# Performance work log

Hardware: AMD Instinct MI355X
Metric: run time of the kernel (lower is better)

Reference implementation:

```python
import jax, jax.numpy as jnp
import numpy as np

D = 128          # node_embed_size
N_NODES = 100000
E = 600000       # edges per relation (3 relations)
NEG_SLOPE = 0.01 # F.leaky_relu default


def setup_inputs() -> dict:
    key = jax.random.key(0)
    ks = jax.random.split(key, 17)
    s = 1.0 / np.sqrt(D)
    inp = {
        "N": jax.random.normal(ks[0], (N_NODES, D), jnp.float32),
        # fc1 weights per domain: [D, D] (torch Linear weight layout: out x in)
        "W1_0": jax.random.normal(ks[1], (D, D), jnp.float32) * s,
        "W1_1": jax.random.normal(ks[2], (D, D), jnp.float32) * s,
        "W1_2": jax.random.normal(ks[3], (D, D), jnp.float32) * s,
        # fc2 weights per domain: [1, 2D]
        "w2_0": jax.random.normal(ks[4], (1, 2 * D), jnp.float32) * s,
        "w2_1": jax.random.normal(ks[5], (1, 2 * D), jnp.float32) * s,
        "w2_2": jax.random.normal(ks[6], (1, 2 * D), jnp.float32) * s,
        "Wq": jax.random.normal(ks[7], (D, D), jnp.float32) * s,
        "Wk": jax.random.normal(ks[8], (D, D), jnp.float32) * s,
        "Wv": jax.random.normal(ks[9], (D, D), jnp.float32) * s,
        "src0": jax.random.randint(ks[10], (E,), 0, N_NODES, jnp.int32),
        "dst0": jax.random.randint(ks[11], (E,), 0, N_NODES, jnp.int32),
        "src1": jax.random.randint(ks[12], (E,), 0, N_NODES, jnp.int32),
        "dst1": jax.random.randint(ks[13], (E,), 0, N_NODES, jnp.int32),
        "src2": jax.random.randint(ks[14], (E,), 0, N_NODES, jnp.int32),
        "dst2": jax.random.randint(ks[15], (E,), 0, N_NODES, jnp.int32),
        "target_idx": 0,
    }
    return inp


def _leaky(x):
    return jnp.where(x >= 0, x, NEG_SLOPE * x)


def _gat_relation(N, W1, w2, src, dst, n_nodes):
    # e_edge = leaky_relu(fc2(cat(fc1(N[src]), fc1(N[dst]))))
    # fc2 on a concat == left half dot src part + right half dot dst part,
    # so compute per-node scores once and gather (standard GAT trick).
    d = N.shape[1]
    h = N @ W1.T                      # [n, d]
    sl = h @ w2[0, :d]                # [n]
    sr = h @ w2[0, d:]                # [n]
    e = _leaky(sl[src] + sr[dst])     # [E]
    # segment softmax over edges grouped by destination node (DGL mailbox softmax)
    m = jax.ops.segment_max(e, dst, num_segments=n_nodes)   # [n], -inf for empty
    ex = jnp.exp(e - m[dst])                                 # [E]
    den = jax.ops.segment_sum(ex, dst, num_segments=n_nodes) # [n]
    alpha = ex / den[dst]                                    # [E]
    # weighted sum of source features; zero for nodes with no in-edges
    return jax.ops.segment_sum(alpha[:, None] * N[src], dst, num_segments=n_nodes)


def reference(N, W1_0, W1_1, W1_2, w2_0, w2_1, w2_2, Wq, Wk, Wv,
              src0, dst0, src1, dst1, src2, dst2, target_idx):
    n, d = N.shape
    rels = [(W1_0, w2_0, src0, dst0), (W1_1, w2_1, src1, dst1), (W1_2, w2_2, src2, dst2)]
    h = [_gat_relation(N, W1, w2, src, dst, n) for (W1, w2, src, dst) in rels]
    hs = jnp.stack(h)                         # [3, n, d]
    q = h[target_idx] @ Wq.T                  # [n, d]
    k = jnp.einsum('knd,ed->kne', hs, Wk)     # [3, n, d]
    # (Wv value is computed in the original but never used in the output)
    e = jnp.einsum('nd,knd->nk', q, k) / jnp.sqrt(jnp.asarray(d, N.dtype))  # [n, 3]
    a = jax.nn.softmax(e, axis=1)             # [n, 3]
    Np = jnp.einsum('nk,knd->nd', a, hs)      # [n, d]
    return Np
```

## Files before the change

kernel.cpp:

```cpp
#include <hip/hip_runtime.h>
#include <hip/hip_bf16.h>
#include <math.h>

#define DD 128

typedef __attribute__((ext_vector_type(8))) short short8;
typedef __attribute__((ext_vector_type(4))) float f32x4;

static __device__ __forceinline__ unsigned short f2bf(float f) {
    unsigned u = __float_as_uint(f);
    u += 0x7fffu + ((u >> 16) & 1u);
    return (unsigned short)(u >> 16);
}
static __device__ __forceinline__ float bflo(unsigned mm) { return __uint_as_float(mm << 16); }
static __device__ __forceinline__ float bfhi(unsigned mm) { return __uint_as_float(mm & 0xffff0000u); }

static __device__ __forceinline__ f32x4 MFMA(short8 a, short8 b, f32x4 c) {
    return __builtin_amdgcn_mfma_f32_16x16x32_bf16(a, b, c, 0, 0, 0);
}
static __device__ __forceinline__ int uswz(int u) { return u ^ ((u >> 4) & 7); }

__global__ void k_fill(float* __restrict__ out, float v, int n) {
    int i = blockIdx.x * 256 + threadIdx.x;
    if (i < n) out[i] = v;
}

__global__ void k_prep(const float* __restrict__ Wq, const float* __restrict__ Wk,
                       const float* __restrict__ W10, const float* __restrict__ W11,
                       const float* __restrict__ W12,
                       const float* __restrict__ w20, const float* __restrict__ w21,
                       const float* __restrict__ w22,
                       unsigned short* __restrict__ Bh, unsigned short* __restrict__ Bl,
                       float* __restrict__ uv, unsigned* __restrict__ cnt, int SEG) {
    int b = blockIdx.x, j = threadIdx.x;
    if (b < DD) {
        float acc = 0.f;
        for (int k = 0; k < DD; ++k)
            acc += Wq[k*DD + b] * Wk[k*DD + j];
        unsigned short hi = f2bf(acc);
        unsigned short lo = f2bf(acc - bflo(hi));
        int t  = j >> 4;
        int ks = b >> 5;
        int l  = ((b >> 3) & 3) * 16 + (j & 15);
        int jj = b & 7;
        int idx = ((t*4 + ks)*64 + l)*8 + jj;
        Bh[idx] = hi;
        Bl[idx] = lo;
    } else if (b < DD + 3) {
        int r = b - DD;
        const float* W1 = (r==0) ? W10 : (r==1 ? W11 : W12);
        const float* w2 = (r==0) ? w20 : (r==1 ? w21 : w22);
        float u = 0.f, v = 0.f;
        for (int k = 0; k < DD; ++k) {
            float w = W1[k*DD + j];
            u += w2[k]      * w;
            v += w2[DD + k] * w;
        }
        uv[r*256 + j]      = u;
        uv[r*256 + DD + j] = v;
    } else {
        int idx = (b - (DD + 3)) * DD + j;
        if (idx < SEG) cnt[idx] = 0u;
    }
}

__global__ void __launch_bounds__(256) k_scores(
        const float* __restrict__ N, const float* __restrict__ uv,
        float* __restrict__ sl, float* __restrict__ sr,
        uint2* __restrict__ Nbf, unsigned* __restrict__ cnt,
        unsigned* __restrict__ rank,
        const int* __restrict__ d0, const int* __restrict__ d1,
        const int* __restrict__ d2,
        int n, int E) {
    int tid = threadIdx.x;
    int g = blockIdx.x * 256 + tid;
    if (g < 3*E) {
        int r = (g >= 2*E) ? 2 : (g >= E ? 1 : 0);
        int e = g - r*E;
        const int* Dd = (r==0) ? d0 : (r==1 ? d1 : d2);
        rank[g] = atomicAdd(&cnt[(size_t)r*n + Dd[e]], 1u);
    }
    int wave = tid >> 6, lane = tid & 63, half = lane >> 5, l32 = lane & 31;
    int iw = blockIdx.x * 8 + wave * 2 + half;
    if (iw >= n && blockIdx.x * 8 >= n) return;
    int i = (iw < n) ? iw : (n - 1);
    float4 nv = ((const float4*)N)[(size_t)i * 32 + l32];
    if (iw < n) {
        uint2 pk;
        pk.x = (unsigned)f2bf(nv.x) | ((unsigned)f2bf(nv.y) << 16);
        pk.y = (unsigned)f2bf(nv.z) | ((unsigned)f2bf(nv.w) << 16);
        Nbf[(size_t)iw * 32 + l32] = pk;
    }
    const float4* UV4 = (const float4*)uv;
    float acc[6];
#pragma unroll
    for (int r = 0; r < 3; ++r) {
        float4 u = UV4[r*64 + l32];
        float4 v = UV4[r*64 + 32 + l32];
        acc[2*r]   = nv.x*u.x + nv.y*u.y + nv.z*u.z + nv.w*u.w;
        acc[2*r+1] = nv.x*v.x + nv.y*v.y + nv.z*v.z + nv.w*v.w;
    }
#pragma unroll
    for (int o = 16; o; o >>= 1) {
#pragma unroll
        for (int q = 0; q < 6; ++q) acc[q] += __shfl_xor(acc[q], o);
    }
    if (l32 == 0 && iw < n) {
#pragma unroll
        for (int r = 0; r < 3; ++r) {
            sl[(size_t)r*n + iw] = acc[2*r];
            sr[(size_t)r*n + iw] = acc[2*r+1];
        }
    }
}

__global__ void __launch_bounds__(256) k_scan1(unsigned* __restrict__ off,
                                               unsigned* __restrict__ bsum, int SEG) {
    __shared__ unsigned s[256];
    int tid = threadIdx.x;
    int i = blockIdx.x * 256 + tid;
    unsigned v = (i < SEG) ? off[i] : 0u;
    s[tid] = v; __syncthreads();
#pragma unroll
    for (int o = 1; o < 256; o <<= 1) {
        unsigned a = (tid >= o) ? s[tid - o] : 0u; __syncthreads();
        s[tid] += a; __syncthreads();
    }
    if (i < SEG) off[i] = s[tid] - v;
    if (tid == 255) bsum[blockIdx.x] = s[255];
}

__global__ void __launch_bounds__(256) k_scan2(unsigned* __restrict__ bsum, int nb) {
    __shared__ unsigned s[256];
    __shared__ unsigned carry;
    int tid = threadIdx.x;
    if (tid == 0) carry = 0u;
    for (int base = 0; base < nb; base += 256) {
        int i = base + tid;
        unsigned v = (i < nb) ? bsum[i] : 0u;
        __syncthreads();
        s[tid] = v; __syncthreads();
#pragma unroll
        for (int o = 1; o < 256; o <<= 1) {
            unsigned a = (tid >= o) ? s[tid - o] : 0u; __syncthreads();
            s[tid] += a; __syncthreads();
        }
        unsigned incl = s[tid], tot = s[255], c = carry;
        if (i < nb) bsum[i] = c + incl - v;
        __syncthreads();
        if (tid == 0) carry = c + tot;
    }
}

__global__ void k_scatter(const int* __restrict__ s0, const int* __restrict__ d0,
                          const int* __restrict__ s1, const int* __restrict__ d1,
                          const int* __restrict__ s2, const int* __restrict__ d2,
                          const float* __restrict__ sl, const float* __restrict__ sr,
                          const unsigned* __restrict__ off,
                          const unsigned* __restrict__ bsum,
                          const unsigned* __restrict__ rank,
                          uint2* __restrict__ edat, int n, int E) {
    int g = blockIdx.x * 256 + threadIdx.x;
    if (g >= 3*E) return;
    int r = (g >= 2*E) ? 2 : (g >= E ? 1 : 0);
    int e = g - r*E;
    const int* S  = (r==0) ? s0 : (r==1 ? s1 : s2);
    const int* Dd = (r==0) ? d0 : (r==1 ? d1 : d2);
    int si = S[e], di = Dd[e];
    int seg = r*n + di;
    float x = sl[(size_t)r*n + si] + sr[seg];
    x = (x >= 0.f) ? x : 0.01f * x;
    unsigned p = off[seg] + bsum[seg >> 8] + rank[g];
    edat[p] = make_uint2((unsigned)si, __float_as_uint(x));
}

__global__ void __launch_bounds__(512, 8) k_node(
        const uint4* __restrict__ Nbf,
        const uint4* __restrict__ B4h, const uint4* __restrict__ B4l,
        const unsigned* __restrict__ off,
        const unsigned* __restrict__ bsum,
        const uint2* __restrict__ edat,
        const int* __restrict__ tgt,
        float* __restrict__ out, int n, int TOT) {
    __shared__ uint4 afrag[2][256];
    __shared__ float Tl[16*132];
    int tid = threadIdx.x;
    int wave = tid >> 6, lane = tid & 63;
    int half = lane >> 5;
    int l32 = lane & 31;
    int g2 = (lane >> 4) & 1;
    int l16 = lane & 15;
    int nid = wave * 2 + half;
    int iw = blockIdx.x * 16 + nid;
    int i = (iw < n) ? iw : (n - 1);
    int t = tgt[0];
    t = (t < 0) ? 0 : (t > 2 ? 2 : t);
    int SEG = 3*n;

    int A[3], C[3];
#pragma unroll
    for (int r = 0; r < 3; ++r) {
        int seg = r*n + i;
        int a = (int)(off[seg] + bsum[seg >> 8]);
        int b = (seg + 1 < SEG) ? (int)(off[seg+1] + bsum[(seg+1) >> 8]) : TOT;
        A[r] = a; C[r] = b - a;
    }

    float m_[3], inv_[3];
#pragma unroll
    for (int r = 0; r < 3; ++r) {
        int cc = C[r];
        float m, s;
        if (cc <= 32) {
            float x = (l32 < cc) ? __uint_as_float(edat[A[r] + l32].y) : -INFINITY;
            m = x;
#pragma unroll
            for (int o = 16; o; o >>= 1) m = fmaxf(m, __shfl_xor(m, o));
            s = (l32 < cc) ? __expf(x - m) : 0.f;
#pragma unroll
            for (int o = 16; o; o >>= 1) s += __shfl_xor(s, o);
        } else {
            m = -INFINITY;
            for (int j = A[r] + l32; j < A[r] + cc; j += 32)
                m = fmaxf(m, __uint_as_float(edat[j].y));
#pragma unroll
            for (int o = 16; o; o >>= 1) m = fmaxf(m, __shfl_xor(m, o));
            s = 0.f;
            for (int j = A[r] + l32; j < A[r] + cc; j += 32)
                s += __expf(__uint_as_float(edat[j].y) - m);
#pragma unroll
            for (int o = 16; o; o >>= 1) s += __shfl_xor(s, o);
        }
        m_[r] = m; inv_[r] = 1.f / s;
    }

    float hr[3][8];
#pragma unroll
    for (int r = 0; r < 3; ++r) {
        float h[8] = {0.f,0.f,0.f,0.f,0.f,0.f,0.f,0.f};
        int cc = C[r], a = A[r];
        float mm = m_[r], iv = inv_[r];
        for (int p = 0; p < cc; p += 4) {
            int i0 = p + g2, i1 = p + 2 + g2;
            int e0 = (i0 < cc) ? i0 : cc - 1;
            int e1 = (i1 < cc) ? i1 : cc - 1;
            uint2 d0 = edat[a + e0];
            uint2 d1 = edat[a + e1];
            uint4 v0 = Nbf[(size_t)d0.x * 16 + l16];
            uint4 v1 = Nbf[(size_t)d1.x * 16 + l16];
            float a0 = (i0 < cc) ? __expf(__uint_as_float(d0.y) - mm) * iv : 0.f;
            float a1 = (i1 < cc) ? __expf(__uint_as_float(d1.y) - mm) * iv : 0.f;
            h[0] += a0*bflo(v0.x) + a1*bflo(v1.x);
            h[1] += a0*bfhi(v0.x) + a1*bfhi(v1.x);
            h[2] += a0*bflo(v0.y) + a1*bflo(v1.y);
            h[3] += a0*bfhi(v0.y) + a1*bfhi(v1.y);
            h[4] += a0*bflo(v0.z) + a1*bflo(v1.z);
            h[5] += a0*bfhi(v0.z) + a1*bfhi(v1.z);
            h[6] += a0*bflo(v0.w) + a1*bflo(v1.w);
            h[7] += a0*bfhi(v0.w) + a1*bfhi(v1.w);
        }
#pragma unroll
        for (int k = 0; k < 8; ++k) {
            h[k] += __shfl_xor(h[k], 16);
            hr[r][k] = h[k];
        }
        if (r == t && l32 < 16) {
            unsigned ph[4], pl[4];
#pragma unroll
            for (int k = 0; k < 4; ++k) {
                unsigned short h0 = f2bf(h[2*k]);
                unsigned short h1 = f2bf(h[2*k+1]);
                unsigned short g0 = f2bf(h[2*k]   - bflo(h0));
                unsigned short g1 = f2bf(h[2*k+1] - bflo(h1));
                ph[k] = (unsigned)h0 | ((unsigned)h1 << 16);
                pl[k] = (unsigned)g0 | ((unsigned)g1 << 16);
            }
            int u = uswz(((l16 >> 2) * 64) + ((l16 & 3) * 16) + nid);
            afrag[0][u] = make_uint4(ph[0], ph[1], ph[2], ph[3]);
            afrag[1][u] = make_uint4(pl[0], pl[1], pl[2], pl[3]);
        }
    }
    __syncthreads();

    {
        int qm = lane >> 4;
        f32x4 acc = {0.f, 0.f, 0.f, 0.f};
        for (int ks = 0; ks < 4; ++ks) {
            uint4 a_hi = afrag[0][uswz(ks*64 + lane)];
            uint4 a_lo = afrag[1][uswz(ks*64 + lane)];
            uint4 b_hi = B4h[(wave*4 + ks)*64 + lane];
            uint4 b_lo = B4l[(wave*4 + ks)*64 + lane];
            acc = MFMA(__builtin_bit_cast(short8, a_hi),
                       __builtin_bit_cast(short8, b_hi), acc);
            acc = MFMA(__builtin_bit_cast(short8, a_lo),
                       __builtin_bit_cast(short8, b_hi), acc);
            acc = MFMA(__builtin_bit_cast(short8, a_hi),
                       __builtin_bit_cast(short8, b_lo), acc);
        }
        int col = wave*16 + l16;
#pragma unroll
        for (int rg = 0; rg < 4; ++rg)
            Tl[(qm*4 + rg)*132 + col] = acc[rg];
    }
    __syncthreads();

    float4 ta = *(const float4*)&Tl[nid*132 + 8*l16];
    float4 tb = *(const float4*)&Tl[nid*132 + 8*l16 + 4];
    float t8[8] = {ta.x, ta.y, ta.z, ta.w, tb.x, tb.y, tb.z, tb.w};

    const float inv = 0.088388347648318447f;
    float e[3];
#pragma unroll
    for (int r = 0; r < 3; ++r) {
        float v = 0.f;
#pragma unroll
        for (int k = 0; k < 8; ++k) v += t8[k]*hr[r][k];
#pragma unroll
        for (int o = 8; o; o >>= 1) v += __shfl_xor(v, o);
        e[r] = v * inv;
    }
    float mx = fmaxf(e[0], fmaxf(e[1], e[2]));
    float x0 = __expf(e[0]-mx), x1 = __expf(e[1]-mx), x2 = __expf(e[2]-mx);
    float sinv = 1.f / (x0 + x1 + x2);
    float aw0 = x0*sinv, aw1 = x1*sinv, aw2 = x2*sinv;
    if (g2 == 0 && iw < n) {
        float4 oa, ob;
        oa.x = aw0*hr[0][0] + aw1*hr[1][0] + aw2*hr[2][0];
        oa.y = aw0*hr[0][1] + aw1*hr[1][1] + aw2*hr[2][1];
        oa.z = aw0*hr[0][2] + aw1*hr[1][2] + aw2*hr[2][2];
        oa.w = aw0*hr[0][3] + aw1*hr[1][3] + aw2*hr[2][3];
        ob.x = aw0*hr[0][4] + aw1*hr[1][4] + aw2*hr[2][4];
        ob.y = aw0*hr[0][5] + aw1*hr[1][5] + aw2*hr[2][5];
        ob.z = aw0*hr[0][6] + aw1*hr[1][6] + aw2*hr[2][6];
        ob.w = aw0*hr[0][7] + aw1*hr[1][7] + aw2*hr[2][7];
        ((float4*)(out + (size_t)iw * DD))[2*l16]     = oa;
        ((float4*)(out + (size_t)iw * DD))[2*l16 + 1] = ob;
    }
}

extern "C" void kernel_launch(void* const* d_in, const int* in_sizes, int n_in,
                              void* d_out, int out_size, void* d_ws, size_t ws_size,
                              hipStream_t stream) {
    float* outp = (float*)d_out;
    int fillgrid = (out_size + 255) / 256;
    if (n_in != 17) {
        k_fill<<<fillgrid, 256, 0, stream>>>(outp, 1024.0f, out_size);
        return;
    }
    int n = in_sizes[0] / DD;
    int E = in_sizes[10];
    bool ok = (in_sizes[0] % DD == 0)
        && in_sizes[1]==DD*DD && in_sizes[2]==DD*DD && in_sizes[3]==DD*DD
        && in_sizes[4]==2*DD  && in_sizes[5]==2*DD  && in_sizes[6]==2*DD
        && in_sizes[7]==DD*DD && in_sizes[8]==DD*DD && in_sizes[9]==DD*DD
        && in_sizes[11]==E && in_sizes[12]==E && in_sizes[13]==E
        && in_sizes[14]==E && in_sizes[15]==E && in_sizes[16]==1;
    if (!ok) {
        k_fill<<<fillgrid, 256, 0, stream>>>(outp, 512.0f, out_size);
        return;
    }
    int SEG = 3*n;
    int NB1 = (SEG + 255) / 256;
    int tot = 3*E;

    size_t o_edat = (size_t)2*SEG + 768 + DD*DD + SEG + NB1 + (size_t)tot;
    o_edat = (o_edat + 1) & ~(size_t)1;
    size_t o_nbf = o_edat + (size_t)2*tot;
    o_nbf = (o_nbf + 3) & ~(size_t)3;
    size_t need_f = o_nbf + (size_t)n*64;
    if (ws_size < need_f * sizeof(float)) {
        k_fill<<<fillgrid, 256, 0, stream>>>(outp, 256.0f, out_size);
        return;
    }

    const float* N   = (const float*)d_in[0];
    const float* W10 = (const float*)d_in[1];
    const float* W11 = (const float*)d_in[2];
    const float* W12 = (const float*)d_in[3];
    const float* w20 = (const float*)d_in[4];
    const float* w21 = (const float*)d_in[5];
    const float* w22 = (const float*)d_in[6];
    const float* Wq  = (const float*)d_in[7];
    const float* Wk  = (const float*)d_in[8];
    const int* s0 = (const int*)d_in[10];
    const int* d0 = (const int*)d_in[11];
    const int* s1 = (const int*)d_in[12];
    const int* d1 = (const int*)d_in[13];
    const int* s2 = (const int*)d_in[14];
    const int* d2 = (const int*)d_in[15];
    const int* tgt = (const int*)d_in[16];

    float* ws = (float*)d_ws;
    float* sl = ws;
    float* sr = sl + SEG;
    float* uv = sr + SEG;
    unsigned short* Bh = (unsigned short*)(uv + 768);
    unsigned short* Bl = Bh + DD*DD;
    unsigned* off  = (unsigned*)(uv + 768 + DD*DD);
    unsigned* bsum = off + SEG;
    unsigned* rank = bsum + NB1;
    uint2*    edat = (uint2*)(ws + o_edat);
    unsigned* Nbf  = (unsigned*)(ws + o_nbf);

    int NBZ = (SEG + DD - 1) / DD;
    int gridS = (n + 7) / 8;
    int gridC = (tot + 255) / 256;
    if (gridC > gridS) gridS = gridC;

    k_prep<<<DD + 3 + NBZ, DD, 0, stream>>>(Wq, Wk, W10, W11, W12,
                                            w20, w21, w22, Bh, Bl, uv, off, SEG);
    k_scores<<<gridS, 256, 0, stream>>>(N, uv, sl, sr, (uint2*)Nbf, off, rank,
                                        d0, d1, d2, n, E);
    k_scan1<<<NB1, 256, 0, stream>>>(off, bsum, SEG);
    k_scan2<<<1, 256, 0, stream>>>(bsum, NB1);
    k_scatter<<<(tot + 255)/256, 256, 0, stream>>>(s0,d0,s1,d1,s2,d2, sl,sr,
                                                   off, bsum, rank, edat, n, E);
    k_node<<<(n + 15)/16, 512, 0, stream>>>((const uint4*)Nbf,
                                            (const uint4*)Bh, (const uint4*)Bl,
                                            off, bsum, edat, tgt, outp, n, tot);
}
```

Before: 394.9 us.

## Map each node to a 16-lane group and halve k_node block size

Result: no change. 388.1 us (-1.7%).

```diff
diff --git a/kernel.cpp b/kernel.cpp
--- a/kernel.cpp
+++ b/kernel.cpp
@@ -174,7 +174,7 @@
     edat[p] = make_uint2((unsigned)si, __float_as_uint(x));
 }
 
-__global__ void __launch_bounds__(512, 8) k_node(
+__global__ void __launch_bounds__(256, 8) k_node(
         const uint4* __restrict__ Nbf,
         const uint4* __restrict__ B4h, const uint4* __restrict__ B4l,
         const unsigned* __restrict__ off,
@@ -186,11 +186,9 @@
     __shared__ float Tl[16*132];
     int tid = threadIdx.x;
     int wave = tid >> 6, lane = tid & 63;
-    int half = lane >> 5;
-    int l32 = lane & 31;
-    int g2 = (lane >> 4) & 1;
+    int grp = lane >> 4;
     int l16 = lane & 15;
-    int nid = wave * 2 + half;
+    int nid = wave * 4 + grp;
     int iw = blockIdx.x * 16 + nid;
     int i = (iw < n) ? iw : (n - 1);
     int t = tgt[0];
@@ -211,25 +209,25 @@
     for (int r = 0; r < 3; ++r) {
         int cc = C[r];
         float m, s;
-        if (cc <= 32) {
-            float x = (l32 < cc) ? __uint_as_float(edat[A[r] + l32].y) : -INFINITY;
+        if (cc <= 16) {
+            float x = (l16 < cc) ? __uint_as_float(edat[A[r] + l16].y) : -INFINITY;
             m = x;
 #pragma unroll
-            for (int o = 16; o; o >>= 1) m = fmaxf(m, __shfl_xor(m, o));
-            s = (l32 < cc) ? __expf(x - m) : 0.f;
-#pragma unroll
-            for (int o = 16; o; o >>= 1) s += __shfl_xor(s, o);
+            for (int o = 8; o; o >>= 1) m = fmaxf(m, __shfl_xor(m, o));
+            s = (l16 < cc) ? __expf(x - m) : 0.f;
+#pragma unroll
+            for (int o = 8; o; o >>= 1) s += __shfl_xor(s, o);
         } else {
             m = -INFINITY;
-            for (int j = A[r] + l32; j < A[r] + cc; j += 32)
+            for (int j = A[r] + l16; j < A[r] + cc; j += 16)
                 m = fmaxf(m, __uint_as_float(edat[j].y));
 #pragma unroll
-            for (int o = 16; o; o >>= 1) m = fmaxf(m, __shfl_xor(m, o));
+            for (int o = 8; o; o >>= 1) m = fmaxf(m, __shfl_xor(m, o));
             s = 0.f;
-            for (int j = A[r] + l32; j < A[r] + cc; j += 32)
+            for (int j = A[r] + l16; j < A[r] + cc; j += 16)
                 s += __expf(__uint_as_float(edat[j].y) - m);
 #pragma unroll
-            for (int o = 16; o; o >>= 1) s += __shfl_xor(s, o);
+            for (int o = 8; o; o >>= 1) s += __shfl_xor(s, o);
         }
         m_[r] = m; inv_[r] = 1.f / s;
     }
@@ -240,16 +238,15 @@
         float h[8] = {0.f,0.f,0.f,0.f,0.f,0.f,0.f,0.f};
         int cc = C[r], a = A[r];
         float mm = m_[r], iv = inv_[r];
-        for (int p = 0; p < cc; p += 4) {
-            int i0 = p + g2, i1 = p + 2 + g2;
-            int e0 = (i0 < cc) ? i0 : cc - 1;
-            int e1 = (i1 < cc) ? i1 : cc - 1;
-            uint2 d0 = edat[a + e0];
+        for (int p = 0; p < cc; p += 2) {
+            int e1 = (p + 1 < cc) ? p + 1 : cc - 1;
+            uint2 d0 = edat[a + p];
             uint2 d1 = edat[a + e1];
             uint4 v0 = Nbf[(size_t)d0.x * 16 + l16];
             uint4 v1 = Nbf[(size_t)d1.x * 16 + l16];
-            float a0 = (i0 < cc) ? __expf(__uint_as_float(d0.y) - mm) * iv : 0.f;
-            float a1 = (i1 < cc) ? __expf(__uint_as_float(d1.y) - mm) * iv : 0.f;
+            float a0 = __expf(__uint_as_float(d0.y) - mm) * iv;
+            float a1 = (p + 1 < cc)
+                ? __expf(__uint_as_float(d1.y) - mm) * iv : 0.f;
             h[0] += a0*bflo(v0.x) + a1*bflo(v1.x);
             h[1] += a0*bfhi(v0.x) + a1*bfhi(v1.x);
             h[2] += a0*bflo(v0.y) + a1*bflo(v1.y);
@@ -260,11 +257,8 @@
             h[7] += a0*bfhi(v0.w) + a1*bfhi(v1.w);
         }
 #pragma unroll
-        for (int k = 0; k < 8; ++k) {
-            h[k] += __shfl_xor(h[k], 16);
-            hr[r][k] = h[k];
-        }
-        if (r == t && l32 < 16) {
+        for (int k = 0; k < 8; ++k) hr[r][k] = h[k];
+        if (r == t) {
             unsigned ph[4], pl[4];
 #pragma unroll
             for (int k = 0; k < 4; ++k) {
@@ -284,23 +278,35 @@
 
     {
         int qm = lane >> 4;
-        f32x4 acc = {0.f, 0.f, 0.f, 0.f};
+        f32x4 acc0 = {0.f, 0.f, 0.f, 0.f};
+        f32x4 acc1 = {0.f, 0.f, 0.f, 0.f};
+        int jt0 = wave*2, jt1 = wave*2 + 1;
         for (int ks = 0; ks < 4; ++ks) {
             uint4 a_hi = afrag[0][uswz(ks*64 + lane)];
             uint4 a_lo = afrag[1][uswz(ks*64 + lane)];
-            uint4 b_hi = B4h[(wave*4 + ks)*64 + lane];
-            uint4 b_lo = B4l[(wave*4 + ks)*64 + lane];
-            acc = MFMA(__builtin_bit_cast(short8, a_hi),
-                       __builtin_bit_cast(short8, b_hi), acc);
-            acc = MFMA(__builtin_bit_cast(short8, a_lo),
-                       __builtin_bit_cast(short8, b_hi), acc);
-            acc = MFMA(__builtin_bit_cast(short8, a_hi),
-                       __builtin_bit_cast(short8, b_lo), acc);
-        }
-        int col = wave*16 + l16;
-#pragma unroll
-        for (int rg = 0; rg < 4; ++rg)
-            Tl[(qm*4 + rg)*132 + col] = acc[rg];
+            uint4 b0h = B4h[(jt0*4 + ks)*64 + lane];
+            uint4 b0l = B4l[(jt0*4 + ks)*64 + lane];
+            uint4 b1h = B4h[(jt1*4 + ks)*64 + lane];
+            uint4 b1l = B4l[(jt1*4 + ks)*64 + lane];
+            acc0 = MFMA(__builtin_bit_cast(short8, a_hi),
+                        __builtin_bit_cast(short8, b0h), acc0);
+            acc1 = MFMA(__builtin_bit_cast(short8, a_hi),
+                        __builtin_bit_cast(short8, b1h), acc1);
+            acc0 = MFMA(__builtin_bit_cast(short8, a_lo),
+                        __builtin_bit_cast(short8, b0h), acc0);
+            acc1 = MFMA(__builtin_bit_cast(short8, a_lo),
+                        __builtin_bit_cast(short8, b1h), acc1);
+            acc0 = MFMA(__builtin_bit_cast(short8, a_hi),
+                        __builtin_bit_cast(short8, b0l), acc0);
+            acc1 = MFMA(__builtin_bit_cast(short8, a_hi),
+                        __builtin_bit_cast(short8, b1l), acc1);
+        }
+        int col0 = jt0*16 + l16, col1 = jt1*16 + l16;
+#pragma unroll
+        for (int rg = 0; rg < 4; ++rg) {
+            Tl[(qm*4 + rg)*132 + col0] = acc0[rg];
+            Tl[(qm*4 + rg)*132 + col1] = acc1[rg];
+        }
     }
     __syncthreads();
 
@@ -323,7 +329,7 @@
     float x0 = __expf(e[0]-mx), x1 = __expf(e[1]-mx), x2 = __expf(e[2]-mx);
     float sinv = 1.f / (x0 + x1 + x2);
     float aw0 = x0*sinv, aw1 = x1*sinv, aw2 = x2*sinv;
-    if (g2 == 0 && iw < n) {
+    if (iw < n) {
         float4 oa, ob;
         oa.x = aw0*hr[0][0] + aw1*hr[1][0] + aw2*hr[2][0];
         oa.y = aw0*hr[0][1] + aw1*hr[1][1] + aw2*hr[2][1];
@@ -415,7 +421,7 @@
     k_scan2<<<1, 256, 0, stream>>>(bsum, NB1);
     k_scatter<<<(tot + 255)/256, 256, 0, stream>>>(s0,d0,s1,d1,s2,d2, sl,sr,
                                                    off, bsum, rank, edat, n, E);
-    k_node<<<(n + 15)/16, 512, 0, stream>>>((const uint4*)Nbf,
+    k_node<<<(n + 15)/16, 256, 0, stream>>>((const uint4*)Nbf,
                                             (const uint4*)Bh, (const uint4*)Bl,
                                             off, bsum, edat, tgt, outp, n, tot);
 }
```
